# Kernel tuning notes

Hardware: AMD Instinct MI355X
Metric: run time of the kernel (lower is better)

The kernel has to match this reference:

```python
import jax, jax.numpy as jnp
import numpy as np

EPS = 1e-06
TEMPERATURE = 1.0
RATIO_WEIGHT = 1.0
ENTROPY_WEIGHT = 0.01


def setup_inputs() -> dict:
    key = jax.random.key(0)
    k1, k2, k3 = jax.random.split(key, 3)
    B, N, C, H = 32, 4096, 256, 256
    x = jax.random.normal(k1, (B, N, C), dtype=jnp.float32)
    W1 = jax.random.normal(k2, (C, H), dtype=jnp.float32) * (1.0 / np.sqrt(C))
    b1 = jnp.zeros((H,), dtype=jnp.float32)
    w2 = jax.random.normal(k3, (H,), dtype=jnp.float32) * (1.0 / np.sqrt(H))
    b2 = jnp.zeros((1,), dtype=jnp.float32)
    return {"x": x, "W1": W1, "b1": b1, "w2": w2, "b2": b2, "k": 16}


def reference(x, W1, b1, w2, b2, k):
    # x: [B, N, C] -> soft-mode TokenGater forward
    N = x.shape[-2]
    # MLP scorer: Linear -> GELU(exact) -> Linear -> squeeze(-1)
    h = jax.nn.gelu(jnp.einsum('bnc,ch->bnh', x, W1) + b1, approximate=False)
    scores = jnp.einsum('bnh,h->bn', h, w2) + b2[0]              # [B, N]
    probs = jax.nn.sigmoid(scores / max(TEMPERATURE, EPS))       # [B, N]

    target_ratio = float(k) / float(max(N, 1))
    ratio = probs.mean(axis=-1)                                  # [B]
    loss_ratio = jnp.mean((ratio - target_ratio) ** 2)
    loss_entropy = jnp.mean(-(probs * jnp.log(probs + EPS)
                              + (1.0 - probs) * jnp.log(1.0 - probs + EPS)))
    aux_loss = RATIO_WEIGHT * loss_ratio + ENTROPY_WEIGHT * loss_entropy

    x_keep = x * probs[..., None]                                # [B, N, C]
    bg_w = 1.0 - probs                                           # [B, N]
    denom = jnp.clip(bg_w.sum(axis=-1, keepdims=True), EPS)      # [B, 1]
    bg = jnp.einsum('bnc,bn->bc', x, bg_w) / denom               # [B, C]
    y = jnp.concatenate([x_keep, bg[..., None, :]], axis=-2)     # [B, N+1, C]
    return (y, aux_loss, scores, probs)
```

## Files before the change

### kernel.cpp

```cpp
#include <hip/hip_runtime.h>
#include <cstdint>

#define GEPS 1e-6f

typedef __attribute__((ext_vector_type(8))) short bf16x8;
typedef __attribute__((ext_vector_type(4))) float f32x4;

__device__ __forceinline__ unsigned short f2bf(float f) {
  unsigned int u = __float_as_uint(f);
  u += 0x7fffu + ((u >> 16) & 1u);
  return (unsigned short)(u >> 16);
}

__device__ __forceinline__ float fast_gelu(float h) {
  float z  = h * 0.70710678118654752f;
  float az = __builtin_fabsf(z);
  float t  = __builtin_amdgcn_rcpf(__builtin_fmaf(0.3275911f, az, 1.0f));
  float poly = t * __builtin_fmaf(t, __builtin_fmaf(t, __builtin_fmaf(t,
               __builtin_fmaf(t, 1.061405429f, -1.453152027f),
               1.421413741f), -0.284496736f), 0.254829592f);
  float e  = __builtin_amdgcn_exp2f(z * z * -1.44269504088896341f);
  float er = __builtin_fmaf(-poly, e, 1.0f);
  er = __builtin_copysignf(er, z);
  float h5 = 0.5f * h;
  return __builtin_fmaf(h5, er, h5);
}

__global__ void pack_w1(const float* __restrict__ W1, unsigned short* __restrict__ wt) {
  int k = blockIdx.x;
  int h = threadIdx.x;
  float v = W1[k * 256 + h];
  int h_tile = h >> 4, tl = h & 15, kk = k >> 5, q = (k >> 3) & 3, j = k & 7;
  wt[(((h_tile << 3) + kk) << 9) + (q << 7) + (tl << 3) + j] = f2bf(v);
}

__global__ __launch_bounds__(256, 5) void gater_main(
    const float* __restrict__ x, const unsigned short* __restrict__ wt,
    const float* __restrict__ b1, const float* __restrict__ w2,
    const float* __restrict__ b2,
    float* __restrict__ y, float* __restrict__ scores, float* __restrict__ probs,
    float* __restrict__ bg_ws, float* __restrict__ sums)
{
  __shared__ short A_lds[64 * 256];
  float* const sc_lds = (float*)A_lds;
  float* const p_lds  = (float*)A_lds + 256;
  float* const bg_lds = (float*)A_lds + 320;

  const int tid = threadIdx.x;
  const int wave = tid >> 6;
  const int tok0 = blockIdx.x * 64;
  const int b = tok0 >> 12;
  const int n0 = tok0 & 4095;
  const float* xblk = x + (size_t)tok0 * 256;
  const float* xt = xblk + tid * 4;

  #pragma unroll
  for (int i = 0; i < 16; ++i) {
    int token = i * 4 + wave;
    const float4 v = *(const float4*)(xt + i * 1024);
    unsigned int lo = (unsigned int)f2bf(v.x) | ((unsigned int)f2bf(v.y) << 16);
    unsigned int hi = (unsigned int)f2bf(v.z) | ((unsigned int)f2bf(v.w) << 16);
    int idx = token * 256 + (((tid & 63) << 2) ^ ((token & 7) << 3));
    *(uint2*)&A_lds[idx] = make_uint2(lo, hi);
  }
  __syncthreads();

  const int lane = tid & 63, tl = lane & 15, q = lane >> 4;

  f32x4 acc[4][4];
  #pragma unroll
  for (int mi = 0; mi < 4; ++mi)
    #pragma unroll
    for (int ni = 0; ni < 4; ++ni)
      acc[mi][ni] = (f32x4){0.f, 0.f, 0.f, 0.f};

  const bf16x8* wtv = (const bf16x8*)wt;
  const int aswz = (tl & 7) << 3;
  #pragma unroll
  for (int kk = 0; kk < 8; ++kk) {
    bf16x8 a[4], bb[4];
    #pragma unroll
    for (int mi = 0; mi < 4; ++mi)
      a[mi] = *(const bf16x8*)&A_lds[(mi * 16 + tl) * 256 + ((kk * 32 + q * 8) ^ aswz)];
    #pragma unroll
    for (int ni = 0; ni < 4; ++ni)
      bb[ni] = wtv[((((wave << 2) + ni) << 3) + kk) * 64 + lane];
    #pragma unroll
    for (int mi = 0; mi < 4; ++mi)
      #pragma unroll
      for (int ni = 0; ni < 4; ++ni)
        acc[mi][ni] = __builtin_amdgcn_mfma_f32_16x16x32_bf16(a[mi], bb[ni], acc[mi][ni], 0, 0, 0);
  }
  __syncthreads();

  float w2v[4], b1v[4];
  #pragma unroll
  for (int ni = 0; ni < 4; ++ni) {
    int h = wave * 64 + ni * 16 + tl;
    w2v[ni] = w2[h];
    b1v[ni] = b1[h];
  }
  #pragma unroll
  for (int mi = 0; mi < 4; ++mi) {
    #pragma unroll
    for (int r = 0; r < 4; ++r) {
      float s = 0.f;
      #pragma unroll
      for (int ni = 0; ni < 4; ++ni) {
        float hv = acc[mi][ni][r] + b1v[ni];
        s += fast_gelu(hv) * w2v[ni];
      }
      #pragma unroll
      for (int m = 1; m < 16; m <<= 1) s += __shfl_xor(s, m, 64);
      if (tl == 0) sc_lds[wave * 64 + mi * 16 + q * 4 + r] = s;
    }
  }
  __syncthreads();

  if (tid < 64) {
    float s = sc_lds[tid] + sc_lds[64 + tid] + sc_lds[128 + tid] + sc_lds[192 + tid] + b2[0];
    float e = __builtin_amdgcn_exp2f(s * -1.44269504088896341f);
    float p = __builtin_amdgcn_rcpf(1.0f + e);
    size_t g = (size_t)tok0 + tid;
    scores[g] = s;
    probs[g] = p;
    p_lds[tid] = p;
    float ent = -(p * logf(p + GEPS) + (1.0f - p) * logf(1.0f - p + GEPS));
    float sp = p, se = ent;
    #pragma unroll
    for (int m = 1; m < 64; m <<= 1) {
      sp += __shfl_xor(sp, m, 64);
      se += __shfl_xor(se, m, 64);
    }
    if (tid == 0) {
      atomicAdd(&sums[b * 2 + 0], sp);
      atomicAdd(&sums[b * 2 + 1], se);
    }
  }
  __syncthreads();

  float* const yt = y + ((size_t)b * 4097 + n0) * 256 + tid * 4;
  float4 bg = make_float4(0.f, 0.f, 0.f, 0.f);
  #pragma unroll
  for (int i = 0; i < 16; ++i) {
    float4 xv = *(const float4*)(xt + i * 1024);
    float p = p_lds[i * 4 + wave];
    f32x4 yv = {xv.x * p, xv.y * p, xv.z * p, xv.w * p};
    __builtin_nontemporal_store(yv, (f32x4*)(yt + i * 1024));
    float bw = 1.0f - p;
    bg.x += xv.x * bw; bg.y += xv.y * bw; bg.z += xv.z * bw; bg.w += xv.w * bw;
  }
  *(float4*)&bg_lds[tid * 4] = bg;
  __syncthreads();
  {
    int c = tid;
    float v = bg_lds[c] + bg_lds[256 + c] + bg_lds[512 + c] + bg_lds[768 + c];
    atomicAdd(&bg_ws[b * 256 + c], v);
  }
}

__global__ void finalize(const float* __restrict__ bg_ws, const float* __restrict__ sums,
                         const int* __restrict__ kp, float* __restrict__ y,
                         float* __restrict__ aux)
{
  int b = blockIdx.x, c = threadIdx.x;
  float sp = sums[b * 2 + 0];
  float denom = fmaxf(4096.0f - sp, GEPS);
  y[((size_t)b * 4097 + 4096) * 256 + c] = bg_ws[b * 256 + c] / denom;
  if (b == 0 && c == 0) {
    float t = (float)kp[0] / 4096.0f;
    float lr = 0.f, le = 0.f;
    for (int i = 0; i < 32; ++i) {
      float r = sums[i * 2 + 0] / 4096.0f;
      lr += (r - t) * (r - t);
      le += sums[i * 2 + 1];
    }
    aux[0] = lr / 32.0f + 0.01f * (le / (32.0f * 4096.0f));
  }
}

extern "C" void kernel_launch(void* const* d_in, const int* in_sizes, int n_in,
                              void* d_out, int out_size, void* d_ws, size_t ws_size,
                              hipStream_t stream) {
  const float* x  = (const float*)d_in[0];
  const float* W1 = (const float*)d_in[1];
  const float* b1 = (const float*)d_in[2];
  const float* w2 = (const float*)d_in[3];
  const float* b2 = (const float*)d_in[4];
  const int*   kp = (const int*)d_in[5];

  float* y = (float*)d_out;
  const size_t Y_ELEMS = (size_t)32 * 4097 * 256;
  float* aux    = y + Y_ELEMS;
  float* scores = aux + 1;
  float* probs  = scores + (size_t)32 * 4096;

  unsigned short* wt = (unsigned short*)d_ws;
  float* bg_ws = (float*)((char*)d_ws + 131072);
  float* sums  = bg_ws + 32 * 256;

  hipMemsetAsync(bg_ws, 0, (32 * 256 + 64) * sizeof(float), stream);
  pack_w1<<<256, 256, 0, stream>>>(W1, wt);
  gater_main<<<2048, 256, 0, stream>>>(x, wt, b1, w2, b2, y, scores, probs, bg_ws, sums);
  finalize<<<32, 256, 0, stream>>>(bg_ws, sums, kp, y, aux);
}
```

Baseline: 339.2 us.

## Fuse finalize into main kernel via last-block counters and vectorize W1 packing

Removes the separate finalize launch. Each batch's last-arriving block, found through an atomic counter after a threadfence, writes the background row, and the last batch block computes the aux loss. The pack_w1 kernel now converts eight K rows per thread and writes them with one 16-byte store, using 32 blocks instead of 256. The y stores switch from nontemporal to regular stores. This adds atomic and fence overhead to every block to save one kernel launch.

```diff
diff --git a/kernel.cpp b/kernel.cpp
--- a/kernel.cpp
+++ b/kernel.cpp
@@ -27,19 +27,24 @@
 }
 
 __global__ void pack_w1(const float* __restrict__ W1, unsigned short* __restrict__ wt) {
-  int k = blockIdx.x;
-  int h = threadIdx.x;
-  float v = W1[k * 256 + h];
-  int h_tile = h >> 4, tl = h & 15, kk = k >> 5, q = (k >> 3) & 3, j = k & 7;
-  wt[(((h_tile << 3) + kk) << 9) + (q << 7) + (tl << 3) + j] = f2bf(v);
+  int h  = threadIdx.x;
+  int k8 = blockIdx.x;
+  int kk = k8 >> 2, q = k8 & 3;
+  int h_tile = h >> 4, tl = h & 15;
+  unsigned short tmp[8];
+  #pragma unroll
+  for (int j = 0; j < 8; ++j)
+    tmp[j] = f2bf(W1[(k8 * 8 + j) * 256 + h]);
+  *(uint4*)&wt[(((h_tile << 3) + kk) << 9) + (q << 7) + (tl << 3)] = *(uint4*)tmp;
 }
 
 __global__ __launch_bounds__(256, 5) void gater_main(
     const float* __restrict__ x, const unsigned short* __restrict__ wt,
     const float* __restrict__ b1, const float* __restrict__ w2,
-    const float* __restrict__ b2,
+    const float* __restrict__ b2, const int* __restrict__ kp,
     float* __restrict__ y, float* __restrict__ scores, float* __restrict__ probs,
-    float* __restrict__ bg_ws, float* __restrict__ sums)
+    float* __restrict__ bg_ws, float* __restrict__ sums,
+    unsigned int* __restrict__ cnt, float* __restrict__ aux)
 {
   __shared__ short A_lds[64 * 256];
   float* const sc_lds = (float*)A_lds;
@@ -145,37 +150,46 @@
   for (int i = 0; i < 16; ++i) {
     float4 xv = *(const float4*)(xt + i * 1024);
     float p = p_lds[i * 4 + wave];
-    f32x4 yv = {xv.x * p, xv.y * p, xv.z * p, xv.w * p};
-    __builtin_nontemporal_store(yv, (f32x4*)(yt + i * 1024));
+    float4 yv = make_float4(xv.x * p, xv.y * p, xv.z * p, xv.w * p);
+    *(float4*)(yt + i * 1024) = yv;
     float bw = 1.0f - p;
     bg.x += xv.x * bw; bg.y += xv.y * bw; bg.z += xv.z * bw; bg.w += xv.w * bw;
   }
   *(float4*)&bg_lds[tid * 4] = bg;
   __syncthreads();
   {
-    int c = tid;
-    float v = bg_lds[c] + bg_lds[256 + c] + bg_lds[512 + c] + bg_lds[768 + c];
-    atomicAdd(&bg_ws[b * 256 + c], v);
-  }
-}
-
-__global__ void finalize(const float* __restrict__ bg_ws, const float* __restrict__ sums,
-                         const int* __restrict__ kp, float* __restrict__ y,
-                         float* __restrict__ aux)
-{
-  int b = blockIdx.x, c = threadIdx.x;
-  float sp = sums[b * 2 + 0];
-  float denom = fmaxf(4096.0f - sp, GEPS);
-  y[((size_t)b * 4097 + 4096) * 256 + c] = bg_ws[b * 256 + c] / denom;
-  if (b == 0 && c == 0) {
-    float t = (float)kp[0] / 4096.0f;
-    float lr = 0.f, le = 0.f;
-    for (int i = 0; i < 32; ++i) {
-      float r = sums[i * 2 + 0] / 4096.0f;
-      lr += (r - t) * (r - t);
-      le += sums[i * 2 + 1];
-    }
-    aux[0] = lr / 32.0f + 0.01f * (le / (32.0f * 4096.0f));
+    float v = bg_lds[tid] + bg_lds[256 + tid] + bg_lds[512 + tid] + bg_lds[768 + tid];
+    atomicAdd(&bg_ws[b * 256 + tid], v);
+  }
+
+  __threadfence();
+  __syncthreads();
+  int* const flag = (int*)sc_lds;
+  float* const spb = (float*)sc_lds + 1;
+  if (tid == 0) {
+    unsigned int old = atomicAdd(&cnt[b], 1u);
+    int last = (old == 63u);
+    flag[0] = last;
+    if (last) spb[0] = atomicAdd(&sums[b * 2 + 0], 0.0f);
+  }
+  __syncthreads();
+  if (flag[0]) {
+    float denom = fmaxf(4096.0f - spb[0], GEPS);
+    float v = atomicAdd(&bg_ws[b * 256 + tid], 0.0f);
+    y[((size_t)b * 4097 + 4096) * 256 + tid] = v / denom;
+    if (tid == 0) {
+      unsigned int oldb = atomicAdd(&cnt[32], 1u);
+      if (oldb == 31u) {
+        float t = (float)kp[0] / 4096.0f;
+        float lr = 0.f, le = 0.f;
+        for (int i = 0; i < 32; ++i) {
+          float r = atomicAdd(&sums[i * 2 + 0], 0.0f) / 4096.0f;
+          lr += (r - t) * (r - t);
+          le += atomicAdd(&sums[i * 2 + 1], 0.0f);
+        }
+        aux[0] = lr / 32.0f + 0.01f * (le / (32.0f * 4096.0f));
+      }
+    }
   }
 }
 
@@ -198,9 +212,10 @@
   unsigned short* wt = (unsigned short*)d_ws;
   float* bg_ws = (float*)((char*)d_ws + 131072);
   float* sums  = bg_ws + 32 * 256;
-
-  hipMemsetAsync(bg_ws, 0, (32 * 256 + 64) * sizeof(float), stream);
-  pack_w1<<<256, 256, 0, stream>>>(W1, wt);
-  gater_main<<<2048, 256, 0, stream>>>(x, wt, b1, w2, b2, y, scores, probs, bg_ws, sums);
-  finalize<<<32, 256, 0, stream>>>(bg_ws, sums, kp, y, aux);
-}
+  unsigned int* cnt = (unsigned int*)(sums + 64);
+
+  hipMemsetAsync(bg_ws, 0, (32 * 256 + 64 + 64) * sizeof(float), stream);
+  pack_w1<<<32, 256, 0, stream>>>(W1, wt);
+  gater_main<<<2048, 256, 0, stream>>>(x, wt, b1, w2, b2, kp,
+                                       y, scores, probs, bg_ws, sums, cnt, aux);
+}
```

Result: slower. 672.6 us (+98.3%).
